# Kernel optimization log

Measured on AMD Instinct MI355X. Metric: run time of the kernel, lower is better.

## Reference

```python
import jax, jax.numpy as jnp
import numpy as np

N = 2000   # nodes
K = 16     # receptive-field size (exact degree incl. self-loop)
C_IN = 16  # input_feats
H = 16     # hidden_size
NC = 18    # num_contractions


def setup_inputs() -> dict:
    key = jax.random.key(0)
    k1, k2, k3, k4, k5, k6 = jax.random.split(key, 6)
    # adjacency with exactly K ones per row (self-loop + K-1 distinct random nbrs)
    u = jax.random.uniform(k1, (N, N))
    u = u.at[jnp.arange(N), jnp.arange(N)].set(-1.0)  # force self into top-K
    nbrs = jnp.argsort(u, axis=1)[:, :K]
    adj = jnp.zeros((N, N), jnp.float32).at[jnp.arange(N)[:, None], nbrs].set(1.0)
    X = jax.random.normal(k2, (N, C_IN), jnp.float32)
    scale = 0.1
    W1 = scale * jax.random.normal(k3, (H, NC * C_IN), jnp.float32)
    b1 = jnp.zeros((H,), jnp.float32)
    W2 = scale * jax.random.normal(k4, (H, NC * H), jnp.float32)
    b2 = jnp.zeros((H,), jnp.float32)
    fc_w = scale * jax.random.normal(k5, (1, 2 * H + C_IN), jnp.float32)
    fc_b = scale * jax.random.normal(k6, (1,), jnp.float32)
    return {"X": X, "adj": adj, "W1": W1, "b1": b1, "W2": W2, "b2": b2,
            "fc_w": fc_w, "fc_b": fc_b}


def _neighbors(adj):
    # each row has exactly K ones -> top_k returns their indices
    _, idx = jax.lax.top_k(adj, K)
    return jnp.sort(idx, axis=1)  # (N, K)


def _contract18(T):
    # T: (n, m, a, b, c) stacked promoted neighbor tensors; 18 contractions 3rd->2nd order
    n, k, _, _, c = T.shape
    tr = lambda M: jnp.swapaxes(M, 1, 2)
    s0, s1, s2 = T.sum(1), T.sum(2), T.sum(3)           # single-index sums
    d0 = jnp.einsum('ixxbc->ixbc', T)                    # diag m=a
    d1 = jnp.einsum('ixaxc->ixac', T)                    # diag m=b
    d2 = jnp.einsum('imyyc->imyc', T)                    # diag a=b
    outs = []
    for M in (s0, s1, s2, d0, d1, d2):
        outs.append(M)
        outs.append(tr(M))                               # 12 so far
    v0, v1, v2 = T.sum((2, 3)), T.sum((1, 3)), T.sum((1, 2))  # double sums -> vectors
    for v in (v0, v1, v2):
        outs.append(jnp.broadcast_to(v[:, :, None, :], (n, k, k, c)))  # rows
        outs.append(jnp.broadcast_to(v[:, None, :, :], (n, k, k, c)))  # cols
    return jnp.concatenate(outs, axis=-1)                # (n, k, k, 18c)


def _forward(X, adj, W1, b1, W2, b2, fc_w, fc_b):
    nbrs = _neighbors(adj)                               # (N, K)
    nbrs_nb = nbrs[nbrs]                                 # (N, K, K)
    # chi[i,m,a,b] = 1 iff a-th member of P_i equals b-th member of P_{nbrs[i,m]}
    chi = (nbrs[:, None, :, None] == nbrs_nb[:, :, None, :]).astype(X.dtype)  # (N,K,K,K)
    # F0: first->second order promotion (features on the diagonal of P_i x P_i)
    F0 = jnp.einsum('ab,iac->iabc', jnp.eye(K, dtype=X.dtype), X[nbrs])  # (N,K,K,C_IN)

    def step(F, W, b):
        Fn = F[nbrs]                                     # (N, m, p, q, c)
        tmp = jnp.einsum('imap,impqc->imaqc', chi, Fn)
        T = jnp.einsum('imaqc,imbq->imabc', tmp, chi)    # promoted + stacked (N,m,a,b,c)
        C = _contract18(T)                               # (N, a, b, 18c)
        return jax.nn.relu(jnp.einsum('iabk,hk->iabh', C, W) + b)

    F1 = step(F0, W1, b1)
    F2 = step(F1, W2, b2)
    g = jnp.concatenate([F0.sum((0, 1, 2)), F1.sum((0, 1, 2)), F2.sum((0, 1, 2))])
    return g @ fc_w.T + fc_b                             # (n_outputs,)


def reference(X, adj, W1, b1, W2, b2, fc_w, fc_b):
    return _forward(X, adj, W1, b1, W2, b2, fc_w, fc_b)
```

## Files before the change

kernel.cpp:

```cpp
#include <hip/hip_runtime.h>

#define NN 2000

typedef _Float16 halfx8 __attribute__((ext_vector_type(8)));
typedef float floatx4 __attribute__((ext_vector_type(4)));

#define LBAR() asm volatile("s_waitcnt lgkmcnt(0)\n\ts_barrier" ::: "memory")

__global__ void build_nbrs_k(const float* __restrict__ adj,
                             int* __restrict__ nbrs) {
    int i = blockIdx.x;
    int lane = threadIdx.x;
    const float* row = adj + (size_t)i * NN;
    float v[32];
#pragma unroll
    for (int c = 0; c < 32; ++c) {
        int col = c * 64 + lane;
        v[c] = (col < NN) ? row[col] : 0.0f;
    }
    int base = 0;
#pragma unroll
    for (int c = 0; c < 32; ++c) {
        bool p = v[c] > 0.5f;
        unsigned long long mask = __ballot(p);
        if (p) {
            int pos = base + __popcll(mask & ((1ull << lane) - 1ull));
            nbrs[i * 16 + pos] = c * 64 + lane;
        }
        base += __popcll(mask);
    }
}

__global__ void build_map_k(const int* __restrict__ nbrs,
                            signed char* __restrict__ map8,
                            signed char* __restrict__ imp8,
                            int4* __restrict__ aux) {
    int idx = blockIdx.x * blockDim.x + threadIdx.x;
    if (idx >= NN * 16) return;
    int i = idx >> 4;
    int m = idx & 15;
    int j = nbrs[idx];
    const int4* pi = (const int4*)(nbrs + (size_t)i * 16);
    const int4* pj = (const int4*)(nbrs + (size_t)j * 16);
    int4 A = pi[0], Bq = pi[1], C = pi[2], D = pi[3];
    int4 E = pj[0], F = pj[1], G = pj[2], H = pj[3];
    int ni[16] = {A.x,A.y,A.z,A.w, Bq.x,Bq.y,Bq.z,Bq.w, C.x,C.y,C.z,C.w, D.x,D.y,D.z,D.w};
    int nj[16] = {E.x,E.y,E.z,E.w, F.x,F.y,F.z,F.w, G.x,G.y,G.z,G.w, H.x,H.y,H.z,H.w};

    int mp[16];
    unsigned long long lo = 0, hi = 0;
#pragma unroll
    for (int a = 0; a < 16; ++a) {
        int r = -1;
#pragma unroll
        for (int p = 0; p < 16; ++p)
            if (nj[p] == ni[a]) r = p;
        mp[a] = r;
        unsigned long long b = (unsigned long long)(r & 0xff);
        if (a < 8) lo |= b << (8 * a); else hi |= b << (8 * (a - 8));
    }
    uint4 pk;
    pk.x = (unsigned)lo; pk.y = (unsigned)(lo >> 32);
    pk.z = (unsigned)hi; pk.w = (unsigned)(hi >> 32);
    *(uint4*)(map8 + ((size_t)idx << 4)) = pk;
    lo = 0; hi = 0;
#pragma unroll
    for (int p = 0; p < 16; ++p) {
        int r = -1;
#pragma unroll
        for (int a = 0; a < 16; ++a)
            if (ni[a] == nj[p]) r = a;
        unsigned long long b = (unsigned long long)(r & 0xff);
        if (p < 8) lo |= b << (8 * p); else hi |= b << (8 * (p - 8));
    }
    pk.x = (unsigned)lo; pk.y = (unsigned)(lo >> 32);
    pk.z = (unsigned)hi; pk.w = (unsigned)(hi >> 32);
    *(uint4*)(imp8 + ((size_t)idx << 4)) = pk;

    unsigned vm = 0;
    int a1 = -1, a2 = -1, pa1 = 0, pa2 = 0;
#pragma unroll
    for (int a = 0; a < 16; ++a) {
        if (mp[a] >= 0) {
            vm |= (1u << a);
            if (a1 < 0)      { a1 = a; pa1 = mp[a]; }
            else if (a2 < 0) { a2 = a; pa2 = mp[a]; }
        }
    }
    int ms = 0;
#pragma unroll
    for (int a = 0; a < 16; ++a)
        if (ni[a] == i) ms = a;
    int4 av;
    av.x = j;
    av.y = (a1 & 0xff) | ((pa1 & 0xff) << 8) | ((a2 & 0xff) << 16) | ((pa2 & 0xff) << 24);
    av.z = (int)(vm | ((unsigned)(mp[m] & 0xff) << 16) | ((unsigned)(ms & 0xff) << 24));
    av.w = 0;
    aux[idx] = av;
}

__global__ void prep_w_k(const float* __restrict__ W1,
                         const float* __restrict__ W2,
                         _Float16* __restrict__ Wpk) {
    int idx = blockIdx.x * blockDim.x + threadIdx.x;
    if (idx >= 2 * 10 * 512) return;
    int stage = idx / 5120;
    int rem = idx % 5120;
    int chunk = rem / 512;
    int r2 = rem % 512;
    int L = r2 / 8, jj = r2 % 8;
    int q = L >> 4, h = L & 15;
    int k = q * 8 + jj;
    const int tA[10] = {2, 6, 10, 0, 14,   3, 7, 11, 1, 15};
    const int tB[10] = {4, 8, -1, 12, 16,  5, 9, -1, 13, 17};
    int tblk = (k < 16) ? tA[chunk] : tB[chunk];
    int c = k & 15;
    const float* W = stage ? W2 : W1;
    float val = (tblk < 0) ? 0.f : W[h * 288 + tblk * 16 + c];
    Wpk[idx] = (_Float16)val;
}

template <int DIAG>
__global__ __launch_bounds__(256, 2)
void step_k(const float* __restrict__ Fp,
            const float* __restrict__ Xp,
            const _Float16* __restrict__ Wpk,
            const float* __restrict__ bias,
            const signed char* __restrict__ map8,
            const signed char* __restrict__ imp8,
            const int4* __restrict__ auxp,
            float* __restrict__ Fout,
            float* __restrict__ gp0,
            float* __restrict__ gp) {
    __shared__ __attribute__((aligned(16))) float S0[16][16][18];
    __shared__ __attribute__((aligned(16))) _Float16 MAP[5][16][16][16];
    __shared__ __attribute__((aligned(16))) float V0f[16][16];
    __shared__ __attribute__((aligned(16))) float V1f[16][16];
    __shared__ __attribute__((aligned(16))) float V2f[16][16];
    __shared__ __attribute__((aligned(16))) float S1f[16][16];

    const int i = blockIdx.x;
    const int t = threadIdx.x;
    const int u = t >> 4;
    const int l = t & 15;
    const int lane = t & 63, q = lane >> 4, h = lane & 15, wv = t >> 6;

    int4 av = auxp[i * 16 + u];
    uint4 imv = *(const uint4*)(imp8 + ((size_t)(i * 16 + u) << 4));
    float bv = bias[l];
    const int j = av.x;
    const int a1 = (int)(signed char)(av.y & 0xff);
    const int pa1 = (av.y >> 8) & 0xff;
    const int a2 = (int)(signed char)((av.y >> 16) & 0xff);
    const int pa2 = (av.y >> 24) & 0xff;
    const unsigned vm = (unsigned)(av.z & 0xffff);
    const int pmm = (av.z >> 16) & 0xff;
    const int ms = (av.z >> 24) & 0xff;

    float frow[16], fcol[16], xv = 0.f;
    if (DIAG) {
        xv = Xp[(size_t)j * 16 + l];
    } else {
        const float* Fi = Fp + (size_t)i * 4096;
#pragma unroll
        for (int b = 0; b < 16; ++b) frow[b] = Fi[(u * 16 + b) * 16 + l];
#pragma unroll
        for (int a = 0; a < 16; ++a) fcol[a] = Fi[(a * 16 + u) * 16 + l];
    }

    float R1[16], R2[16];
    if (!DIAG && u != ms) {
        const float* P1 = Fp + (((size_t)j * 256 + pa1 * 16) * 16) + l;
#pragma unroll
        for (int p = 0; p < 16; ++p) R1[p] = P1[p * 16];
        if (a2 >= 0) {
            const float* P2 = Fp + (((size_t)j * 256 + pa2 * 16) * 16) + l;
#pragma unroll
            for (int p = 0; p < 16; ++p) R2[p] = P2[p * 16];
        }
    }
    halfx8 B[10];
    {
        const halfx8* Wp8 = (const halfx8*)Wpk;
#pragma unroll
        for (int c = 0; c < 10; ++c) B[c] = Wp8[c * 64 + lane];
    }

    if (u != ms) {
        uint4 z = {0u, 0u, 0u, 0u};
#pragma unroll
        for (int k = 0; k < 5; ++k) {
            *(uint4*)&MAP[k][u][l][0] = z;
            *(uint4*)&MAP[k][u][l][8] = z;
        }
    }
    if (DIAG) {
        S1f[u][l] = xv;
        V1f[u][l] = xv;
        V2f[u][l] = xv;
#pragma unroll
        for (int b = 0; b < 16; ++b) S0[u][b][l] = (b == u) ? xv : 0.f;
        MAP[0][ms][u][l] = (_Float16)xv;
        MAP[1][ms][u][l] = (_Float16)xv;
        _Float16 dz = (_Float16)((u == ms) ? xv : 0.f);
        MAP[2][ms][u][l] = dz;
        MAP[3][ms][u][l] = dz;
        MAP[4][ms][u][l] = (_Float16)xv;
    } else {
        float s2 = 0.f, a10 = 0.f, a8 = 0.f;
#pragma unroll
        for (int b = 0; b < 16; ++b) {
            float v = frow[b];
            s2 += v;
            S0[u][b][l] = v;
            if (b == u)  a10 = v;
            if (b == ms) a8 = v;
        }
        float s1 = 0.f, a6 = 0.f;
#pragma unroll
        for (int a = 0; a < 16; ++a) {
            float v = fcol[a];
            s1 += v;
            if (a == ms) a6 = v;
        }
        S1f[u][l] = s2;
        V1f[u][l] = s2;
        V2f[u][l] = s1;
        MAP[0][ms][u][l] = (_Float16)s1;
        MAP[1][ms][u][l] = (_Float16)s2;
        MAP[2][ms][u][l] = (_Float16)a6;
        MAP[3][ms][u][l] = (_Float16)a8;
        MAP[4][ms][u][l] = (_Float16)a10;
    }
    LBAR();

    if (u != ms) {
        const int m = u;
        float v0acc = 0.f;
        if (DIAG) {
#pragma unroll
            for (int a = 0; a < 16; ++a) {
                if ((vm >> a) & 1u) {
                    float v = S1f[a][l];
                    v0acc += v;
                    atomicAdd(&S0[a][a][l], v);
                    atomicAdd(&V1f[a][l], v);
                    atomicAdd(&V2f[a][l], v);
                    MAP[0][m][a][l] = (_Float16)v;
                    MAP[1][m][a][l] = (_Float16)v;
                    MAP[4][m][a][l] = (_Float16)v;
                    if (a == m) { MAP[2][m][m][l] = (_Float16)v; MAP[3][m][m][l] = (_Float16)v; }
                }
            }
        } else {
            float colacc[16];
#pragma unroll
            for (int p = 0; p < 16; ++p) colacc[p] = 0.f;
            auto process = [&](int a, int pa, const float (&vr)[16]) {
                float rowacc = 0.f, a8v = 0.f, a10v = 0.f;
                const bool am = (a == m);
#pragma unroll
                for (int p = 0; p < 16; ++p) {
                    float v = vr[p];
                    if (p == pmm) a8v = v;
                    if (p == pa)  a10v = v;
                    unsigned dw = (p < 4) ? imv.x : ((p < 8) ? imv.y : ((p < 12) ? imv.z : imv.w));
                    int b = (int)(signed char)((dw >> (8 * (p & 3))) & 0xffu);
                    if (b >= 0) {
                        rowacc += v;
                        colacc[p] += v;
                        atomicAdd(&S0[a][b][l], v);
                        atomicAdd(&V2f[b][l], v);
                        if (am) MAP[2][m][b][l] = (_Float16)v;
                    }
                }
                v0acc += rowacc;
                atomicAdd(&V1f[a][l], rowacc);
                MAP[1][m][a][l] = (_Float16)rowacc;
                MAP[3][m][a][l] = (_Float16)a8v;
                MAP[4][m][a][l] = (_Float16)a10v;
            };
            process(a1, pa1, R1);
            if (a2 >= 0) process(a2, pa2, R2);
            unsigned rm = vm & ~(1u << a1);
            if (a2 >= 0) rm &= ~(1u << a2);
            if (rm) {
                uint4 mpq = *(const uint4*)(map8 + ((size_t)(i * 16 + u) << 4));
                do {
                    int a = __builtin_ctz(rm); rm &= rm - 1;
                    unsigned dw = (a & 8) ? ((a & 4) ? mpq.w : mpq.z) : ((a & 4) ? mpq.y : mpq.x);
                    int pa = (int)(signed char)((dw >> (8 * (a & 3))) & 0xffu);
                    float RT[16];
                    const float* P3 = Fp + (((size_t)j * 256 + pa * 16) * 16) + l;
#pragma unroll
                    for (int p = 0; p < 16; ++p) RT[p] = P3[p * 16];
                    process(a, pa, RT);
                } while (rm);
            }
#pragma unroll
            for (int p = 0; p < 16; ++p) {
                unsigned dw = (p < 4) ? imv.x : ((p < 8) ? imv.y : ((p < 12) ? imv.z : imv.w));
                int b = (int)(signed char)((dw >> (8 * (p & 3))) & 0xffu);
                if (b >= 0) MAP[0][m][b][l] = (_Float16)colacc[p];
            }
        }
        V0f[m][l] = v0acc;
    } else {
        float v0s = 0.f;
#pragma unroll
        for (int b = 0; b < 16; ++b) v0s += S1f[b][l];
        V0f[ms][l] = v0s;
        if (DIAG) gp0[(size_t)i * 16 + l] = v0s;
    }

    floatx4 acc1[4], acc2[4];
#pragma unroll
    for (int tt = 0; tt < 4; ++tt) {
        acc1[tt] = (floatx4){0.f, 0.f, 0.f, 0.f};
        acc2[tt] = (floatx4){0.f, 0.f, 0.f, 0.f};
    }
    halfx8 az;
#pragma unroll
    for (int z = 0; z < 8; ++z) az[z] = (_Float16)0.f;
    const int wbase = wv * 4;
#pragma unroll
    for (int tt = 0; tt < 4; ++tt) {
        const int x = wbase + tt;
        halfx8 p0, p1, p2;
        if (q < 2) {
            p0 = *(const halfx8*)&MAP[0][x][h][q * 8];
            p1 = *(const halfx8*)&MAP[2][x][h][q * 8];
            p2 = *(const halfx8*)&MAP[4][x][h][q * 8];
        } else {
            const int c0 = (q - 2) * 8;
            p0 = *(const halfx8*)&MAP[1][x][h][c0];
            p1 = *(const halfx8*)&MAP[3][x][h][c0];
            p2 = az;
        }
        acc1[tt] = __builtin_amdgcn_mfma_f32_16x16x32_f16(p0, B[0], acc1[tt], 0, 0, 0);
        acc1[tt] = __builtin_amdgcn_mfma_f32_16x16x32_f16(p1, B[1], acc1[tt], 0, 0, 0);
        acc1[tt] = __builtin_amdgcn_mfma_f32_16x16x32_f16(p2, B[2], acc1[tt], 0, 0, 0);
        acc2[tt] = __builtin_amdgcn_mfma_f32_16x16x32_f16(p0, B[5], acc2[tt], 0, 0, 0);
        acc2[tt] = __builtin_amdgcn_mfma_f32_16x16x32_f16(p1, B[6], acc2[tt], 0, 0, 0);
        acc2[tt] = __builtin_amdgcn_mfma_f32_16x16x32_f16(p2, B[7], acc2[tt], 0, 0, 0);
    }
    LBAR();

    auto cvt8 = [](const float* p) -> halfx8 {
        float2 fa = *(const float2*)p, fb = *(const float2*)(p + 2),
               fc = *(const float2*)(p + 4), fd = *(const float2*)(p + 6);
        halfx8 r;
        r[0] = (_Float16)fa.x; r[1] = (_Float16)fa.y; r[2] = (_Float16)fb.x; r[3] = (_Float16)fb.y;
        r[4] = (_Float16)fc.x; r[5] = (_Float16)fc.y; r[6] = (_Float16)fd.x; r[7] = (_Float16)fd.y;
        return r;
    };
    auto cvt8a = [](const float* p) -> halfx8 {
        float4 va = *(const float4*)p, vb = *(const float4*)(p + 4);
        halfx8 r;
        r[0] = (_Float16)va.x; r[1] = (_Float16)va.y; r[2] = (_Float16)va.z; r[3] = (_Float16)va.w;
        r[4] = (_Float16)vb.x; r[5] = (_Float16)vb.y; r[6] = (_Float16)vb.z; r[7] = (_Float16)vb.w;
        return r;
    };
#pragma unroll
    for (int tt = 0; tt < 4; ++tt) {
        const int x = wbase + tt;
        halfx8 p3, p4;
        if (q < 2) {
            p3 = cvt8(&S0[x][h][q * 8]);
            p4 = cvt8a(&V1f[x][q * 8]);
        } else {
            const int c0 = (q - 2) * 8;
            p3 = cvt8a(&V0f[x][c0]);
            p4 = cvt8a(&V2f[x][c0]);
        }
        acc1[tt] = __builtin_amdgcn_mfma_f32_16x16x32_f16(p3, B[3], acc1[tt], 0, 0, 0);
        acc1[tt] = __builtin_amdgcn_mfma_f32_16x16x32_f16(p4, B[4], acc1[tt], 0, 0, 0);
        acc2[tt] = __builtin_amdgcn_mfma_f32_16x16x32_f16(p3, B[8], acc2[tt], 0, 0, 0);
        acc2[tt] = __builtin_amdgcn_mfma_f32_16x16x32_f16(p4, B[9], acc2[tt], 0, 0, 0);
    }
    LBAR();

    float* P2f = &S0[0][0][0];
#pragma unroll
    for (int tt = 0; tt < 4; ++tt) {
        const int x = wbase + tt;
#pragma unroll
        for (int r = 0; r < 4; ++r)
            P2f[(x * 16 + (q * 4 + r)) * 17 + h] = acc2[tt][r];
    }
    LBAR();

    float gpart = 0.f;
#pragma unroll
    for (int tt = 0; tt < 4; ++tt) {
        const int x = wbase + tt;
#pragma unroll
        for (int r = 0; r < 4; ++r) {
            const int y = q * 4 + r;
            float val = acc1[tt][r] + P2f[(y * 16 + x) * 17 + h] + bv;
            val = fmaxf(val, 0.f);
            gpart += val;
            if (Fout) Fout[(size_t)i * 4096 + (x * 16 + y) * 16 + h] = val;
        }
    }
    gpart += __shfl_xor(gpart, 16, 64);
    gpart += __shfl_xor(gpart, 32, 64);
    if (lane < 16) gp[((size_t)i * 4 + wv) * 16 + h] = gpart;
}

__global__ void reduce_g_k(const float* __restrict__ parts,
                           float* __restrict__ gsum) {
    int r = blockIdx.x;
    int h = r & 15;
    const float* p;
    int cnt;
    if (r < 16)      { p = parts + h;                     cnt = NN; }
    else if (r < 32) { p = parts + NN * 16 + h;           cnt = NN * 4; }
    else             { p = parts + NN * 16 + NN * 64 + h; cnt = NN * 4; }
    int t = threadIdx.x;
    float s = 0.f;
    for (int n = t; n < cnt; n += 256) s += p[(size_t)n * 16];
#pragma unroll
    for (int off = 32; off > 0; off >>= 1) s += __shfl_xor(s, off, 64);
    __shared__ float wsum[4];
    if ((t & 63) == 0) wsum[t >> 6] = s;
    __syncthreads();
    if (t == 0) gsum[r] = wsum[0] + wsum[1] + wsum[2] + wsum[3];
}

__global__ void finalize_k(const float* __restrict__ gsum,
                           const float* __restrict__ fcw,
                           const float* __restrict__ fcb,
                           float* __restrict__ out) {
    int t = threadIdx.x;
    float v = (t < 48) ? gsum[t] * fcw[t] : 0.f;
#pragma unroll
    for (int off = 32; off > 0; off >>= 1) v += __shfl_xor(v, off, 64);
    if (t == 0) out[0] = v + fcb[0];
}

extern "C" void kernel_launch(void* const* d_in, const int* in_sizes, int n_in,
                              void* d_out, int out_size, void* d_ws, size_t ws_size,
                              hipStream_t stream) {
    const float* X   = (const float*)d_in[0];
    const float* adj = (const float*)d_in[1];
    const float* W1  = (const float*)d_in[2];
    const float* b1  = (const float*)d_in[3];
    const float* W2  = (const float*)d_in[4];
    const float* b2  = (const float*)d_in[5];
    const float* fcw = (const float*)d_in[6];
    const float* fcb = (const float*)d_in[7];
    float* out = (float*)d_out;
    char* ws = (char*)d_ws;

    float*       gsum  = (float*)(ws + 0);
    int*         nbrs  = (int*)(ws + 1024);
    signed char* map8  = (signed char*)(ws + 129280);
    signed char* imp8  = (signed char*)(ws + 641280);
    int4*        aux   = (int4*)(ws + 1153280);
    float*       parts = (float*)(ws + 1665280);
    _Float16*    Wpk   = (_Float16*)(ws + 2817280);
    float*       F1    = (float*)(ws + 2837760);

    build_nbrs_k<<<NN, 64, 0, stream>>>(adj, nbrs);
    build_map_k<<<(NN * 16 + 255) / 256, 256, 0, stream>>>(nbrs, map8, imp8, aux);
    prep_w_k<<<40, 256, 0, stream>>>(W1, W2, Wpk);
    step_k<1><<<NN, 256, 0, stream>>>(nullptr, X, Wpk, b1, map8, imp8, aux, F1,
                                      parts, parts + (size_t)NN * 16);
    step_k<0><<<NN, 256, 0, stream>>>(F1, X, Wpk + 5120, b2, map8, imp8, aux, nullptr,
                                      nullptr, parts + (size_t)NN * 16 + (size_t)NN * 64);
    reduce_g_k<<<48, 256, 0, stream>>>(parts, gsum);
    finalize_k<<<1, 64, 0, stream>>>(gsum, fcw, fcb, out);
}
```

Before: 165.1 us.

## Fuse neighbor-map and weight-packing prep kernels into first step kernel

```diff
diff --git a/kernel.cpp b/kernel.cpp
--- a/kernel.cpp
+++ b/kernel.cpp
@@ -31,104 +31,16 @@
     }
 }
 
-__global__ void build_map_k(const int* __restrict__ nbrs,
-                            signed char* __restrict__ map8,
-                            signed char* __restrict__ imp8,
-                            int4* __restrict__ aux) {
-    int idx = blockIdx.x * blockDim.x + threadIdx.x;
-    if (idx >= NN * 16) return;
-    int i = idx >> 4;
-    int m = idx & 15;
-    int j = nbrs[idx];
-    const int4* pi = (const int4*)(nbrs + (size_t)i * 16);
-    const int4* pj = (const int4*)(nbrs + (size_t)j * 16);
-    int4 A = pi[0], Bq = pi[1], C = pi[2], D = pi[3];
-    int4 E = pj[0], F = pj[1], G = pj[2], H = pj[3];
-    int ni[16] = {A.x,A.y,A.z,A.w, Bq.x,Bq.y,Bq.z,Bq.w, C.x,C.y,C.z,C.w, D.x,D.y,D.z,D.w};
-    int nj[16] = {E.x,E.y,E.z,E.w, F.x,F.y,F.z,F.w, G.x,G.y,G.z,G.w, H.x,H.y,H.z,H.w};
-
-    int mp[16];
-    unsigned long long lo = 0, hi = 0;
-#pragma unroll
-    for (int a = 0; a < 16; ++a) {
-        int r = -1;
-#pragma unroll
-        for (int p = 0; p < 16; ++p)
-            if (nj[p] == ni[a]) r = p;
-        mp[a] = r;
-        unsigned long long b = (unsigned long long)(r & 0xff);
-        if (a < 8) lo |= b << (8 * a); else hi |= b << (8 * (a - 8));
-    }
-    uint4 pk;
-    pk.x = (unsigned)lo; pk.y = (unsigned)(lo >> 32);
-    pk.z = (unsigned)hi; pk.w = (unsigned)(hi >> 32);
-    *(uint4*)(map8 + ((size_t)idx << 4)) = pk;
-    lo = 0; hi = 0;
-#pragma unroll
-    for (int p = 0; p < 16; ++p) {
-        int r = -1;
-#pragma unroll
-        for (int a = 0; a < 16; ++a)
-            if (ni[a] == nj[p]) r = a;
-        unsigned long long b = (unsigned long long)(r & 0xff);
-        if (p < 8) lo |= b << (8 * p); else hi |= b << (8 * (p - 8));
-    }
-    pk.x = (unsigned)lo; pk.y = (unsigned)(lo >> 32);
-    pk.z = (unsigned)hi; pk.w = (unsigned)(hi >> 32);
-    *(uint4*)(imp8 + ((size_t)idx << 4)) = pk;
-
-    unsigned vm = 0;
-    int a1 = -1, a2 = -1, pa1 = 0, pa2 = 0;
-#pragma unroll
-    for (int a = 0; a < 16; ++a) {
-        if (mp[a] >= 0) {
-            vm |= (1u << a);
-            if (a1 < 0)      { a1 = a; pa1 = mp[a]; }
-            else if (a2 < 0) { a2 = a; pa2 = mp[a]; }
-        }
-    }
-    int ms = 0;
-#pragma unroll
-    for (int a = 0; a < 16; ++a)
-        if (ni[a] == i) ms = a;
-    int4 av;
-    av.x = j;
-    av.y = (a1 & 0xff) | ((pa1 & 0xff) << 8) | ((a2 & 0xff) << 16) | ((pa2 & 0xff) << 24);
-    av.z = (int)(vm | ((unsigned)(mp[m] & 0xff) << 16) | ((unsigned)(ms & 0xff) << 24));
-    av.w = 0;
-    aux[idx] = av;
-}
-
-__global__ void prep_w_k(const float* __restrict__ W1,
-                         const float* __restrict__ W2,
-                         _Float16* __restrict__ Wpk) {
-    int idx = blockIdx.x * blockDim.x + threadIdx.x;
-    if (idx >= 2 * 10 * 512) return;
-    int stage = idx / 5120;
-    int rem = idx % 5120;
-    int chunk = rem / 512;
-    int r2 = rem % 512;
-    int L = r2 / 8, jj = r2 % 8;
-    int q = L >> 4, h = L & 15;
-    int k = q * 8 + jj;
-    const int tA[10] = {2, 6, 10, 0, 14,   3, 7, 11, 1, 15};
-    const int tB[10] = {4, 8, -1, 12, 16,  5, 9, -1, 13, 17};
-    int tblk = (k < 16) ? tA[chunk] : tB[chunk];
-    int c = k & 15;
-    const float* W = stage ? W2 : W1;
-    float val = (tblk < 0) ? 0.f : W[h * 288 + tblk * 16 + c];
-    Wpk[idx] = (_Float16)val;
-}
-
 template <int DIAG>
 __global__ __launch_bounds__(256, 2)
 void step_k(const float* __restrict__ Fp,
             const float* __restrict__ Xp,
-            const _Float16* __restrict__ Wpk,
+            const float* __restrict__ Wsrc,
             const float* __restrict__ bias,
-            const signed char* __restrict__ map8,
-            const signed char* __restrict__ imp8,
-            const int4* __restrict__ auxp,
+            const int* __restrict__ nbrs,
+            signed char* __restrict__ map8,
+            signed char* __restrict__ imp8,
+            int4* __restrict__ auxp,
             float* __restrict__ Fout,
             float* __restrict__ gp0,
             float* __restrict__ gp) {
@@ -138,6 +50,8 @@
     __shared__ __attribute__((aligned(16))) float V1f[16][16];
     __shared__ __attribute__((aligned(16))) float V2f[16][16];
     __shared__ __attribute__((aligned(16))) float S1f[16][16];
+    __shared__ __attribute__((aligned(16))) signed char IMPB[16][16];
+    __shared__ __attribute__((aligned(16))) signed char MPB[16][16];
 
     const int i = blockIdx.x;
     const int t = threadIdx.x;
@@ -145,22 +59,69 @@
     const int l = t & 15;
     const int lane = t & 63, q = lane >> 4, h = lane & 15, wv = t >> 6;
 
-    int4 av = auxp[i * 16 + u];
-    uint4 imv = *(const uint4*)(imp8 + ((size_t)(i * 16 + u) << 4));
+    halfx8 az;
+#pragma unroll
+    for (int z = 0; z < 8; ++z) az[z] = (_Float16)0.f;
+
+    halfx8 Bf[10];
+    {
+        const int tAq[10] = {2, 6, 10, 0, 14, 3, 7, 11, 1, 15};
+        const int tBq[10] = {4, 8, -1, 12, 16, 5, 9, -1, 13, 17};
+#pragma unroll
+        for (int c2 = 0; c2 < 10; ++c2) {
+            int tb = (q < 2) ? tAq[c2] : tBq[c2];
+            if (tb < 0) { Bf[c2] = az; continue; }
+            const float* wp = Wsrc + h * 288 + tb * 16 + (q & 1) * 8;
+            float4 va = *(const float4*)wp, vb = *(const float4*)(wp + 4);
+            halfx8 r;
+            r[0] = (_Float16)va.x; r[1] = (_Float16)va.y; r[2] = (_Float16)va.z; r[3] = (_Float16)va.w;
+            r[4] = (_Float16)vb.x; r[5] = (_Float16)vb.y; r[6] = (_Float16)vb.z; r[7] = (_Float16)vb.w;
+            Bf[c2] = r;
+        }
+    }
     float bv = bias[l];
-    const int j = av.x;
-    const int a1 = (int)(signed char)(av.y & 0xff);
-    const int pa1 = (av.y >> 8) & 0xff;
-    const int a2 = (int)(signed char)((av.y >> 16) & 0xff);
-    const int pa2 = (av.y >> 24) & 0xff;
-    const unsigned vm = (unsigned)(av.z & 0xffff);
-    const int pmm = (av.z >> 16) & 0xff;
-    const int ms = (av.z >> 24) & 0xff;
-
-    float frow[16], fcol[16], xv = 0.f;
+
+    int j, ms = 0;
+    unsigned vm = 0;
+    int a1 = -1, pa1 = 0, a2 = -1, pa2 = 0, pmm = 0;
+    uint4 imv;
+    float xv = 0.f;
+    float frow[16], fcol[16];
+
     if (DIAG) {
+        j = nbrs[(size_t)i * 16 + u];
+        const int4* nbp = (const int4*)(nbrs + (size_t)i * 16);
+        int4 nA = nbp[0], nB = nbp[1], nC = nbp[2], nD = nbp[3];
+        int nbreg[16] = {nA.x,nA.y,nA.z,nA.w, nB.x,nB.y,nB.z,nB.w,
+                         nC.x,nC.y,nC.z,nC.w, nD.x,nD.y,nD.z,nD.w};
+        const int4* njp = (const int4*)(nbrs + (size_t)j * 16);
+        int4 mA = njp[0], mB = njp[1], mC = njp[2], mD = njp[3];
+        int njreg[16] = {mA.x,mA.y,mA.z,mA.w, mB.x,mB.y,mB.z,mB.w,
+                         mC.x,mC.y,mC.z,mC.w, mD.x,mD.y,mD.z,mD.w};
         xv = Xp[(size_t)j * 16 + l];
+#pragma unroll
+        for (int a = 0; a < 16; ++a)
+            if (nbreg[a] == i) ms = a;
+        int impl = -1, mpl = -1;
+#pragma unroll
+        for (int a = 0; a < 16; ++a)
+            if (nbreg[a] == njreg[l]) impl = a;
+#pragma unroll
+        for (int p = 0; p < 16; ++p)
+            if (njreg[p] == nbreg[l]) mpl = p;
+        IMPB[u][l] = (signed char)impl;
+        MPB[u][l]  = (signed char)mpl;
     } else {
+        int4 av = auxp[i * 16 + u];
+        imv = *(const uint4*)(imp8 + ((size_t)(i * 16 + u) << 4));
+        j   = av.x;
+        a1  = (int)(signed char)(av.y & 0xff);
+        pa1 = (av.y >> 8) & 0xff;
+        a2  = (int)(signed char)((av.y >> 16) & 0xff);
+        pa2 = (av.y >> 24) & 0xff;
+        vm  = (unsigned)(av.z & 0xffff);
+        pmm = (av.z >> 16) & 0xff;
+        ms  = (av.z >> 24) & 0xff;
         const float* Fi = Fp + (size_t)i * 4096;
 #pragma unroll
         for (int b = 0; b < 16; ++b) frow[b] = Fi[(u * 16 + b) * 16 + l];
@@ -178,12 +139,6 @@
 #pragma unroll
             for (int p = 0; p < 16; ++p) R2[p] = P2[p * 16];
         }
-    }
-    halfx8 B[10];
-    {
-        const halfx8* Wp8 = (const halfx8*)Wpk;
-#pragma unroll
-        for (int c = 0; c < 10; ++c) B[c] = Wp8[c * 64 + lane];
     }
 
     if (u != ms) {
@@ -233,6 +188,35 @@
         MAP[4][ms][u][l] = (_Float16)a10;
     }
     LBAR();
+
+    if (DIAG) {
+        uint4 mpq = *(const uint4*)&MPB[u][0];
+        imv = *(const uint4*)&IMPB[u][0];
+#pragma unroll
+        for (int a = 0; a < 16; ++a) {
+            unsigned dw = (a < 4) ? mpq.x : ((a < 8) ? mpq.y : ((a < 12) ? mpq.z : mpq.w));
+            int pa = (int)(signed char)((dw >> (8 * (a & 3))) & 0xffu);
+            if (pa >= 0) {
+                vm |= (1u << a);
+                if (a1 < 0)      { a1 = a; pa1 = pa; }
+                else if (a2 < 0) { a2 = a; pa2 = pa; }
+            }
+        }
+        {
+            unsigned dw = (u & 8) ? ((u & 4) ? mpq.w : mpq.z) : ((u & 4) ? mpq.y : mpq.x);
+            pmm = (int)(signed char)((dw >> (8 * (u & 3))) & 0xffu);
+        }
+        if (l == 0) {
+            *(uint4*)(map8 + ((size_t)(i * 16 + u) << 4)) = mpq;
+            *(uint4*)(imp8 + ((size_t)(i * 16 + u) << 4)) = imv;
+            int4 av;
+            av.x = j;
+            av.y = (a1 & 0xff) | ((pa1 & 0xff) << 8) | ((a2 & 0xff) << 16) | ((pa2 & 0xff) << 24);
+            av.z = (int)(vm | ((unsigned)(pmm & 0xff) << 16) | ((unsigned)(ms & 0xff) << 24));
+            av.w = 0;
+            auxp[i * 16 + u] = av;
+        }
+    }
 
     if (u != ms) {
         const int m = u;
@@ -319,9 +303,6 @@
         acc1[tt] = (floatx4){0.f, 0.f, 0.f, 0.f};
         acc2[tt] = (floatx4){0.f, 0.f, 0.f, 0.f};
     }
-    halfx8 az;
-#pragma unroll
-    for (int z = 0; z < 8; ++z) az[z] = (_Float16)0.f;
     const int wbase = wv * 4;
 #pragma unroll
     for (int tt = 0; tt < 4; ++tt) {
@@ -337,12 +318,12 @@
             p1 = *(const halfx8*)&MAP[3][x][h][c0];
             p2 = az;
         }
-        acc1[tt] = __builtin_amdgcn_mfma_f32_16x16x32_f16(p0, B[0], acc1[tt], 0, 0, 0);
-        acc1[tt] = __builtin_amdgcn_mfma_f32_16x16x32_f16(p1, B[1], acc1[tt], 0, 0, 0);
-        acc1[tt] = __builtin_amdgcn_mfma_f32_16x16x32_f16(p2, B[2], acc1[tt], 0, 0, 0);
-        acc2[tt] = __builtin_amdgcn_mfma_f32_16x16x32_f16(p0, B[5], acc2[tt], 0, 0, 0);
-        acc2[tt] = __builtin_amdgcn_mfma_f32_16x16x32_f16(p1, B[6], acc2[tt], 0, 0, 0);
-        acc2[tt] = __builtin_amdgcn_mfma_f32_16x16x32_f16(p2, B[7], acc2[tt], 0, 0, 0);
+        acc1[tt] = __builtin_amdgcn_mfma_f32_16x16x32_f16(p0, Bf[0], acc1[tt], 0, 0, 0);
+        acc1[tt] = __builtin_amdgcn_mfma_f32_16x16x32_f16(p1, Bf[1], acc1[tt], 0, 0, 0);
+        acc1[tt] = __builtin_amdgcn_mfma_f32_16x16x32_f16(p2, Bf[2], acc1[tt], 0, 0, 0);
+        acc2[tt] = __builtin_amdgcn_mfma_f32_16x16x32_f16(p0, Bf[5], acc2[tt], 0, 0, 0);
+        acc2[tt] = __builtin_amdgcn_mfma_f32_16x16x32_f16(p1, Bf[6], acc2[tt], 0, 0, 0);
+        acc2[tt] = __builtin_amdgcn_mfma_f32_16x16x32_f16(p2, Bf[7], acc2[tt], 0, 0, 0);
     }
     LBAR();
 
@@ -373,14 +354,13 @@
             p3 = cvt8a(&V0f[x][c0]);
             p4 = cvt8a(&V2f[x][c0]);
         }
-        acc1[tt] = __builtin_amdgcn_mfma_f32_16x16x32_f16(p3, B[3], acc1[tt], 0, 0, 0);
-        acc1[tt] = __builtin_amdgcn_mfma_f32_16x16x32_f16(p4, B[4], acc1[tt], 0, 0, 0);
-        acc2[tt] = __builtin_amdgcn_mfma_f32_16x16x32_f16(p3, B[8], acc2[tt], 0, 0, 0);
-        acc2[tt] = __builtin_amdgcn_mfma_f32_16x16x32_f16(p4, B[9], acc2[tt], 0, 0, 0);
-    }
-    LBAR();
-
-    float* P2f = &S0[0][0][0];
+        acc1[tt] = __builtin_amdgcn_mfma_f32_16x16x32_f16(p3, Bf[3], acc1[tt], 0, 0, 0);
+        acc1[tt] = __builtin_amdgcn_mfma_f32_16x16x32_f16(p4, Bf[4], acc1[tt], 0, 0, 0);
+        acc2[tt] = __builtin_amdgcn_mfma_f32_16x16x32_f16(p3, Bf[8], acc2[tt], 0, 0, 0);
+        acc2[tt] = __builtin_amdgcn_mfma_f32_16x16x32_f16(p4, Bf[9], acc2[tt], 0, 0, 0);
+    }
+
+    float* P2f = (float*)&MAP[0][0][0][0];
 #pragma unroll
     for (int tt = 0; tt < 4; ++tt) {
         const int x = wbase + tt;
@@ -459,15 +439,12 @@
     signed char* imp8  = (signed char*)(ws + 641280);
     int4*        aux   = (int4*)(ws + 1153280);
     float*       parts = (float*)(ws + 1665280);
-    _Float16*    Wpk   = (_Float16*)(ws + 2817280);
-    float*       F1    = (float*)(ws + 2837760);
+    float*       F1    = (float*)(ws + 2817280);
 
     build_nbrs_k<<<NN, 64, 0, stream>>>(adj, nbrs);
-    build_map_k<<<(NN * 16 + 255) / 256, 256, 0, stream>>>(nbrs, map8, imp8, aux);
-    prep_w_k<<<40, 256, 0, stream>>>(W1, W2, Wpk);
-    step_k<1><<<NN, 256, 0, stream>>>(nullptr, X, Wpk, b1, map8, imp8, aux, F1,
+    step_k<1><<<NN, 256, 0, stream>>>(nullptr, X, W1, b1, nbrs, map8, imp8, aux, F1,
                                       parts, parts + (size_t)NN * 16);
-    step_k<0><<<NN, 256, 0, stream>>>(F1, X, Wpk + 5120, b2, map8, imp8, aux, nullptr,
+    step_k<0><<<NN, 256, 0, stream>>>(F1, X, W2, b2, nbrs, map8, imp8, aux, nullptr,
                                       nullptr, parts + (size_t)NN * 16 + (size_t)NN * 64);
     reduce_g_k<<<48, 256, 0, stream>>>(parts, gsum);
     finalize_k<<<1, 64, 0, stream>>>(gsum, fcw, fcb, out);
```

Result: slower. 188.0 us (+13.9%).
